# Performance work log

Measured on AMD Instinct MI355X. Metric: run time of the kernel, lower is better.

## Reference

```python
import jax, jax.numpy as jnp
import numpy as np

B, C, H, W = 32, 256, 32, 32
K, HEADS, U, V = 16, 4, 1, 64  # dim_depth, heads, dim_u, dim_v = dim_out//heads
R = 23
PAD = (R - 1) // 2
EPS = 1e-5


def setup_inputs() -> dict:
    key = jax.random.key(0)
    ks = jax.random.split(key, 10)
    return {
        "x": jax.random.normal(ks[0], (B, C, H, W), jnp.float32),
        "Wq": jax.random.normal(ks[1], (K * HEADS, C), jnp.float32) * (1.0 / np.sqrt(C)),
        "bn_q_w": jax.random.uniform(ks[2], (K * HEADS,), jnp.float32, 0.5, 1.5),
        "bn_q_b": jax.random.normal(ks[3], (K * HEADS,), jnp.float32) * 0.1,
        "Wk": jax.random.normal(ks[4], (K * U, C), jnp.float32) * (1.0 / np.sqrt(C)),
        "Wv": jax.random.normal(ks[5], (V * U, C), jnp.float32) * (1.0 / np.sqrt(C)),
        "bn_v_w": jax.random.uniform(ks[6], (V * U,), jnp.float32, 0.5, 1.5),
        "bn_v_b": jax.random.normal(ks[7], (V * U,), jnp.float32) * 0.1,
        "embedding": jax.random.normal(ks[8], (K, U, 1, R, R), jnp.float32),
        "gamma": jax.random.normal(ks[9], (1,), jnp.float32),
    }


def _conv1x1(x, w):
    # x: [b,c,h,w], w: [o,c] -> [b,o,h,w]
    return jnp.einsum('bchw,oc->bohw', x, w)


def _bn(x, w, b):
    # training-mode BatchNorm2d: batch stats over (b,h,w) per channel
    mean = jnp.mean(x, axis=(0, 2, 3), keepdims=True)
    var = jnp.var(x, axis=(0, 2, 3), keepdims=True)
    xn = (x - mean) * jax.lax.rsqrt(var + EPS)
    return xn * w[None, :, None, None] + b[None, :, None, None]


def reference(x, Wq, bn_q_w, bn_q_b, Wk, Wv, bn_v_w, bn_v_b, embedding, gamma):
    b, c, h, w = x.shape
    n = h * w
    queries = _bn(_conv1x1(x, Wq), bn_q_w, bn_q_b).reshape(b, HEADS, K, n)        # bhkn
    softmax = jax.nn.softmax(_conv1x1(x, Wk).reshape(b, K, U, n), axis=-1)         # bkun
    values = _bn(_conv1x1(x, Wv), bn_v_w, bn_v_b).reshape(b, V, U, n)              # bvun

    # content lambda
    lambda_c = jnp.einsum('bkun,bvun->bkv', softmax, values)
    y_c = jnp.einsum('bhkn,bkv->bhvn', queries, lambda_c)

    # position lambda via conv3d over (V, H, W) with kernel (1, R, R)
    v5 = jnp.transpose(values, (0, 2, 1, 3)).reshape(b, U, V, h, w)                # NCDHW, C=U, D=V
    lambda_p = jax.lax.conv_general_dilated(
        v5, embedding,
        window_strides=(1, 1, 1),
        padding=((0, 0), (PAD, PAD), (PAD, PAD)),
        dimension_numbers=('NCDHW', 'OIDHW', 'NCDHW'))                              # [b,K,V,h,w]
    lambda_p = lambda_p.reshape(b, K, V, n)
    y_p = jnp.einsum('bhkn,bkvn->bhvn', queries, lambda_p)

    out = (y_c + y_p).reshape(b, HEADS * V, h, w)
    out = out + gamma * out
    return out
```

## Files before the change

kernel.cpp:

```cpp
#include <hip/hip_runtime.h>
#include <math.h>

#define BB 32
#define CC 256
#define NPIX 1024
#define KD 16
#define NHEADS 4
#define VDIM 64
#define RR 23
#define PADR 11
#define EPSBN 1e-5f
#define NCH 16

typedef short short8v __attribute__((ext_vector_type(8)));
typedef short short4v __attribute__((ext_vector_type(4)));
typedef float floatx4 __attribute__((ext_vector_type(4)));

__device__ __forceinline__ unsigned short f2bf(float f) {
  union { float f; unsigned u; } c; c.f = f;
  unsigned u = c.u;
  return (unsigned short)((u + 0x7FFFu + ((u >> 16) & 1u)) >> 16);
}
__device__ __forceinline__ float bf2f(unsigned short h) {
  union { unsigned u; float f; } c; c.u = ((unsigned)h) << 16;
  return c.f;
}

__global__ __launch_bounds__(256) void k_prep(const float* __restrict__ emb,
    unsigned short* __restrict__ embA,
    const float* __restrict__ Wq, const float* __restrict__ Wk,
    const float* __restrict__ Wv, unsigned short* __restrict__ wA) {
  int bid = blockIdx.x;
  if (bid < 46) {
    int l = bid * 256 + threadIdx.x;
    if (l >= 23 * 16 * 32) return;
    int dr = l >> 9, rem = l & 511;
    int m = rem >> 5, kd = rem & 31;
    unsigned short val = 0;
    if (kd < 23) val = f2bf(emb[(size_t)m * 529 + dr * 23 + kd]);
    embA[l] = val;
  } else {
    int idx = (bid - 46) * 256 + threadIdx.x;
    int j = idx & 7, lane = (idx >> 3) & 63, ks = (idx >> 9) & 7, ot = idx >> 12;
    int o = ot * 16 + (lane & 15);
    int c = ks * 32 + (lane >> 4) * 8 + j;
    const float* src = (o < 64) ? (Wq + (size_t)o * CC)
                     : (o < 80) ? (Wk + (size_t)(o - 64) * CC)
                                : (Wv + (size_t)(o - 80) * CC);
    wA[idx] = f2bf(src[c]);
  }
}

__global__ __launch_bounds__(256) void k_proj(const float* __restrict__ x,
    const unsigned short* __restrict__ wA,
    float* __restrict__ q_pre, float* __restrict__ k_pre, float* __restrict__ v_pre) {
  int b = blockIdx.y;
  int t = threadIdx.x;
  int s = t >> 6;
  int lane = t & 63;
  int nl = lane & 15, quad = lane >> 4;
  int pix = blockIdx.x * 64 + s * 16 + nl;

  const float* xb = x + ((size_t)b * CC) * NPIX + pix;
  const unsigned short* ap = wA + lane * 8;

  floatx4 acc[9];
#pragma unroll
  for (int i = 0; i < 9; ++i) acc[i] = (floatx4){0.f, 0.f, 0.f, 0.f};

#pragma unroll
  for (int ks = 0; ks < 8; ++ks) {
    union { short8v v; unsigned short u[8]; } bb;
    const float* xc = xb + ((size_t)(ks * 32 + quad * 8)) * NPIX;
#pragma unroll
    for (int j = 0; j < 8; ++j) bb.u[j] = f2bf(xc[(size_t)j * NPIX]);
#pragma unroll
    for (int ot = 0; ot < 9; ++ot) {
      short8v af = *(const short8v*)(ap + ((ot * 8 + ks) << 9));
      acc[ot] = __builtin_amdgcn_mfma_f32_16x16x32_bf16(af, bb.v, acc[ot], 0, 0, 0);
    }
  }

#pragma unroll
  for (int ot = 0; ot < 9; ++ot) {
#pragma unroll
    for (int r = 0; r < 4; ++r) {
      int o = ot * 16 + quad * 4 + r;
      float val = acc[ot][r];
      if (o < 64)      q_pre[((size_t)b * 64 + o) * NPIX + pix] = val;
      else if (o < 80) k_pre[((size_t)b * 16 + (o - 64)) * NPIX + pix] = val;
      else             v_pre[((size_t)b * 64 + (o - 80)) * NPIX + pix] = val;
    }
  }
}

__global__ __launch_bounds__(256) void k_bnstats(const float* __restrict__ q_pre,
    const float* __restrict__ v_pre,
    const float* __restrict__ bn_q_w, const float* __restrict__ bn_q_b,
    const float* __restrict__ bn_v_w, const float* __restrict__ bn_v_b,
    float* __restrict__ stats) {
  int ch = blockIdx.x;
  bool isq = ch < 64;
  int c = isq ? ch : ch - 64;
  const float* src = (isq ? q_pre : v_pre) + (size_t)c * NPIX;
  float s = 0.f, ss = 0.f;
  for (int idx = threadIdx.x; idx < BB * NPIX; idx += 256) {
    int bb = idx >> 10, nn = idx & 1023;
    float v = src[(size_t)bb * 64 * NPIX + nn];
    s += v; ss = fmaf(v, v, ss);
  }
#pragma unroll
  for (int off = 32; off > 0; off >>= 1) {
    s += __shfl_down(s, off);
    ss += __shfl_down(ss, off);
  }
  __shared__ float sh[8];
  if ((threadIdx.x & 63) == 0) {
    sh[(threadIdx.x >> 6) * 2] = s;
    sh[(threadIdx.x >> 6) * 2 + 1] = ss;
  }
  __syncthreads();
  if (threadIdx.x == 0) {
    s = sh[0] + sh[2] + sh[4] + sh[6];
    ss = sh[1] + sh[3] + sh[5] + sh[7];
    const float inv = 1.0f / (float)(BB * NPIX);
    float mean = s * inv;
    float var = ss * inv - mean * mean;
    float rstd = rsqrtf(var + EPSBN);
    float w = isq ? bn_q_w[c] : bn_v_w[c];
    float bi = isq ? bn_q_b[c] : bn_v_b[c];
    float scale = rstd * w;
    float shift = bi - mean * scale;
    if (isq) { stats[c] = scale; stats[64 + c] = shift; }
    else     { stats[128 + c] = scale; stats[192 + c] = shift; }
  }
}

__global__ __launch_bounds__(256) void k_nvsm(float* __restrict__ vn,
    const float* __restrict__ stats, float* __restrict__ vnT,
    const float* __restrict__ k_pre, float* __restrict__ p) {
  __shared__ float lds[64 * 65];
  __shared__ float shm[4], shs[4];
  int b = blockIdx.y, bx = blockIdx.x, t = threadIdx.x;
  if (bx < 16) {
    int n0 = bx * 64;
    for (int l = t; l < 4096; l += 256) {
      int o = l >> 6, nn = l & 63;
      size_t a = ((size_t)b * 64 + o) * NPIX + n0 + nn;
      float v = fmaf(vn[a], stats[128 + o], stats[192 + o]);
      vn[a] = v;
      lds[o * 65 + nn] = v;
    }
    __syncthreads();
    for (int l = t; l < 4096; l += 256) {
      int nn = l >> 6, o = l & 63;
      vnT[((size_t)b * NPIX + n0 + nn) * 64 + o] = lds[o * 65 + nn];
    }
  } else {
    int k = bx - 16;
    const float* src = k_pre + ((size_t)b * 16 + k) * NPIX;
    float v[4];
    float mx = -1e30f;
#pragma unroll
    for (int i = 0; i < 4; ++i) { v[i] = src[t + 256 * i]; mx = fmaxf(mx, v[i]); }
#pragma unroll
    for (int off = 32; off > 0; off >>= 1) mx = fmaxf(mx, __shfl_down(mx, off));
    if ((t & 63) == 0) shm[t >> 6] = mx;
    __syncthreads();
    mx = fmaxf(fmaxf(shm[0], shm[1]), fmaxf(shm[2], shm[3]));
    float s = 0.f;
#pragma unroll
    for (int i = 0; i < 4; ++i) { v[i] = __expf(v[i] - mx); s += v[i]; }
#pragma unroll
    for (int off = 32; off > 0; off >>= 1) s += __shfl_down(s, off);
    if ((t & 63) == 0) shs[t >> 6] = s;
    __syncthreads();
    float r = 1.0f / (shs[0] + shs[1] + shs[2] + shs[3]);
    float* dst = p + ((size_t)b * 16 + k) * NPIX;
#pragma unroll
    for (int i = 0; i < 4; ++i) dst[t + 256 * i] = v[i] * r;
  }
}

__global__ __launch_bounds__(256) void k_lambda_p(const float* __restrict__ p,
    const float* __restrict__ vnT, float* __restrict__ lcp) {
  __shared__ float pl[16 * 64];
  int b = blockIdx.y, nc = blockIdx.x, t = threadIdx.x;
  int n0 = nc * 64;
  for (int l = t; l < 1024; l += 256) {
    int k = l >> 6, nn = l & 63;
    pl[l] = p[((size_t)b * 16 + k) * NPIX + n0 + nn];
  }
  __syncthreads();
  int v = t & 63, wg = t >> 6;
  const float* vt = vnT + ((size_t)b * NPIX + n0) * 64 + v;
  float acc[4] = {0.f, 0.f, 0.f, 0.f};
  for (int i = 0; i < 64; ++i) {
    float val = vt[(size_t)i * 64];
#pragma unroll
    for (int j = 0; j < 4; ++j)
      acc[j] = fmaf(pl[(wg * 4 + j) * 64 + i], val, acc[j]);
  }
  float* dst = lcp + ((size_t)(b * NCH + nc) * 16) * 64;
#pragma unroll
  for (int j = 0; j < 4; ++j)
    dst[(size_t)(wg * 4 + j) * 64 + v] = acc[j];
}

#define IMG_RS 68
#define IMG_CS 3728
#define LAM_RS 1032

union KMainLDS {
  short imgc[4 * IMG_CS];
  short lam[16 * LAM_RS];
};

__device__ __forceinline__ short8v ld_win(const short* p) {
  union { short8v s8; short4v s4[2]; } bu;
  bu.s4[0] = *(const short4v*)p;
  bu.s4[1] = *(const short4v*)(p + 4);
  return bu.s8;
}

__global__ __launch_bounds__(256, 3) void k_conv(const float* __restrict__ vn,
    const float* __restrict__ lcp, const unsigned short* __restrict__ embA,
    unsigned short* __restrict__ lamG) {
  __shared__ __align__(16) KMainLDS u;
  __shared__ float lcv[16];
  int b = blockIdx.y, v = blockIdx.x, t = threadIdx.x;

  int4* z4 = (int4*)u.imgc;
  for (int l = t; l < 1864; l += 256) z4[l] = make_int4(0, 0, 0, 0);
  if (t < 16) {
    float s = 0.f;
#pragma unroll
    for (int nc = 0; nc < NCH; ++nc)
      s += lcp[(((size_t)b * NCH + nc) * 16 + t) * 64 + v];
    lcv[t] = s;
  }
  __syncthreads();

  const float* vsrc = vn + ((size_t)b * 64 + v) * NPIX;
  for (int l = t; l < 512; l += 256) {
    int pix = l * 2;
    int y = pix >> 5, xx = pix & 31;
    float2 vv = *(const float2*)(vsrc + pix);
    unsigned short h0 = f2bf(vv.x), h1 = f2bf(vv.y);
#pragma unroll
    for (int s = 0; s < 4; ++s) {
      int base = s * IMG_CS + (y + PADR) * IMG_RS + xx + PADR + s;
      u.imgc[base] = (short)h0;
      u.imgc[base + 1] = (short)h1;
    }
  }
  __syncthreads();

  int lane = t & 63, wv = t >> 6;
  int nl = lane & 15, quad = lane >> 4;
  int y0 = wv * 8;
  int scopy = (4 - (nl & 3)) & 3;
  int colbase = scopy * IMG_CS + nl + quad * 8 + scopy;
  const unsigned short* aptr = embA + nl * 32 + quad * 8;

  floatx4 acc[16];
#pragma unroll
  for (int i = 0; i < 16; ++i) acc[i] = (floatx4){0.f, 0.f, 0.f, 0.f};

  short8v bfrag[8][2];
#pragma unroll
  for (int rr = 0; rr < 8; ++rr) {
    const short* rp = &u.imgc[(y0 + rr) * IMG_RS + colbase];
    bfrag[rr][0] = ld_win(rp);
    bfrag[rr][1] = ld_win(rp + 16);
  }

  short8v a0 = *(const short8v*)aptr;
  short8v a1 = *(const short8v*)(aptr + 512);
#pragma unroll
  for (int dr = 0; dr < RR; ++dr) {
    short8v afrag = a0;
    a0 = a1;
    if (dr < RR - 2) a1 = *(const short8v*)(aptr + (dr + 2) * 512);
#pragma unroll
    for (int rr = 0; rr < 8; ++rr) {
      int slot = (dr + rr) & 7;
      acc[rr * 2 + 0] = __builtin_amdgcn_mfma_f32_16x16x32_bf16(afrag, bfrag[slot][0], acc[rr * 2 + 0], 0, 0, 0);
      acc[rr * 2 + 1] = __builtin_amdgcn_mfma_f32_16x16x32_bf16(afrag, bfrag[slot][1], acc[rr * 2 + 1], 0, 0, 0);
    }
    if (dr < RR - 1) {
      const short* rp = &u.imgc[(y0 + dr + 8) * IMG_RS + colbase];
      int slot = dr & 7;
      bfrag[slot][0] = ld_win(rp);
      bfrag[slot][1] = ld_win(rp + 16);
    }
  }

  __syncthreads();
#pragma unroll
  for (int tt = 0; tt < 16; ++tt) {
    int y = y0 + (tt >> 1), c0 = (tt & 1) << 4;
    int pix = y * 32 + c0 + nl;
#pragma unroll
    for (int r = 0; r < 4; ++r)
      u.lam[(quad * 4 + r) * LAM_RS + pix] = (short)f2bf(acc[tt][r] + lcv[quad * 4 + r]);
  }
  __syncthreads();

  uint4* dst = (uint4*)(lamG + ((size_t)(b * 64 + v)) * 16 * 1024);
  for (int idx = t; idx < 2048; idx += 256) {
    int row = idx >> 7, col = idx & 127;
    dst[row * 128 + col] = *(const uint4*)&u.lam[row * LAM_RS + col * 8];
  }
}

__global__ __launch_bounds__(256) void k_epi2(const unsigned short* __restrict__ lamG,
    const float* __restrict__ q_pre, const float* __restrict__ stats,
    const float* __restrict__ gamma, float* __restrict__ out) {
  __shared__ float qs[64 * 64];
  int b = blockIdx.y, nc = blockIdx.x, z = blockIdx.z, t = threadIdx.x;
  int n0 = nc * 64;
  for (int l = t; l < 4096; l += 256) {
    int o = l >> 6, nn = l & 63;
    qs[l] = fmaf(q_pre[((size_t)b * 64 + o) * NPIX + n0 + nn], stats[o], stats[64 + o]);
  }
  __syncthreads();
  float g1 = 1.0f + gamma[0];
  int p0 = (t & 15) * 4;
  int g = t >> 4;
#pragma unroll
  for (int vi = 0; vi < 2; ++vi) {
    int v = z * 32 + vi * 16 + g;
    const unsigned short* ls = lamG + ((size_t)(b * 64 + v)) * 16 * 1024 + n0 + p0;
    float yacc[4][4];
#pragma unroll
    for (int h = 0; h < 4; ++h)
#pragma unroll
      for (int i = 0; i < 4; ++i) yacc[h][i] = 0.f;
#pragma unroll
    for (int k = 0; k < 16; ++k) {
      uint2 w = *(const uint2*)(ls + k * 1024);
      float l0 = bf2f((unsigned short)(w.x & 0xffffu));
      float l1 = bf2f((unsigned short)(w.x >> 16));
      float l2 = bf2f((unsigned short)(w.y & 0xffffu));
      float l3 = bf2f((unsigned short)(w.y >> 16));
#pragma unroll
      for (int h = 0; h < 4; ++h) {
        const float* qrow = &qs[(h * 16 + k) * 64 + p0];
        yacc[h][0] = fmaf(qrow[0], l0, yacc[h][0]);
        yacc[h][1] = fmaf(qrow[1], l1, yacc[h][1]);
        yacc[h][2] = fmaf(qrow[2], l2, yacc[h][2]);
        yacc[h][3] = fmaf(qrow[3], l3, yacc[h][3]);
      }
    }
#pragma unroll
    for (int h = 0; h < 4; ++h) {
      float4 r;
      r.x = g1 * yacc[h][0]; r.y = g1 * yacc[h][1];
      r.z = g1 * yacc[h][2]; r.w = g1 * yacc[h][3];
      *(float4*)&out[((size_t)b * 256 + h * 64 + v) * NPIX + n0 + p0] = r;
    }
  }
}

__global__ __launch_bounds__(256, 3) void k_fused(const float* __restrict__ vn,
    const float* __restrict__ q_pre, const float* __restrict__ stats,
    const float* __restrict__ lcp, const unsigned short* __restrict__ embA,
    const float* __restrict__ gamma, float* __restrict__ out) {
  __shared__ __align__(16) KMainLDS u;
  __shared__ float lcv[16];
  int b = blockIdx.y, v = blockIdx.x, t = threadIdx.x;

  int4* z4 = (int4*)u.imgc;
  for (int l = t; l < 1864; l += 256) z4[l] = make_int4(0, 0, 0, 0);
  if (t < 16) {
    float s = 0.f;
#pragma unroll
    for (int nc = 0; nc < NCH; ++nc)
      s += lcp[(((size_t)b * NCH + nc) * 16 + t) * 64 + v];
    lcv[t] = s;
  }
  __syncthreads();

  const float* vsrc = vn + ((size_t)b * 64 + v) * NPIX;
  for (int l = t; l < 512; l += 256) {
    int pix = l * 2;
    int y = pix >> 5, xx = pix & 31;
    float2 vv = *(const float2*)(vsrc + pix);
    unsigned short h0 = f2bf(vv.x), h1 = f2bf(vv.y);
#pragma unroll
    for (int s = 0; s < 4; ++s) {
      int base = s * IMG_CS + (y + PADR) * IMG_RS + xx + PADR + s;
      u.imgc[base] = (short)h0;
      u.imgc[base + 1] = (short)h1;
    }
  }
  __syncthreads();

  int lane = t & 63, wv = t >> 6;
  int nl = lane & 15, quad = lane >> 4;
  int y0 = wv * 8;
  int scopy = (4 - (nl & 3)) & 3;
  int colbase = scopy * IMG_CS + nl + quad * 8 + scopy;
  const unsigned short* aptr = embA + nl * 32 + quad * 8;

  floatx4 acc[16];
#pragma unroll
  for (int i = 0; i < 16; ++i) acc[i] = (floatx4){0.f, 0.f, 0.f, 0.f};

  short8v bfrag[8][2];
#pragma unroll
  for (int rr = 0; rr < 8; ++rr) {
    const short* rp = &u.imgc[(y0 + rr) * IMG_RS + colbase];
    bfrag[rr][0] = ld_win(rp);
    bfrag[rr][1] = ld_win(rp + 16);
  }

  short8v a0 = *(const short8v*)aptr;
  short8v a1 = *(const short8v*)(aptr + 512);
#pragma unroll
  for (int dr = 0; dr < RR; ++dr) {
    short8v afrag = a0;
    a0 = a1;
    if (dr < RR - 2) a1 = *(const short8v*)(aptr + (dr + 2) * 512);
#pragma unroll
    for (int rr = 0; rr < 8; ++rr) {
      int slot = (dr + rr) & 7;
      acc[rr * 2 + 0] = __builtin_amdgcn_mfma_f32_16x16x32_bf16(afrag, bfrag[slot][0], acc[rr * 2 + 0], 0, 0, 0);
      acc[rr * 2 + 1] = __builtin_amdgcn_mfma_f32_16x16x32_bf16(afrag, bfrag[slot][1], acc[rr * 2 + 1], 0, 0, 0);
    }
    if (dr < RR - 1) {
      const short* rp = &u.imgc[(y0 + dr + 8) * IMG_RS + colbase];
      int slot = dr & 7;
      bfrag[slot][0] = ld_win(rp);
      bfrag[slot][1] = ld_win(rp + 16);
    }
  }

  __syncthreads();
#pragma unroll
  for (int tt = 0; tt < 16; ++tt) {
    int y = y0 + (tt >> 1), c0 = (tt & 1) << 4;
    int pix = y * 32 + c0 + nl;
#pragma unroll
    for (int r = 0; r < 4; ++r)
      u.lam[(quad * 4 + r) * LAM_RS + pix] = (short)f2bf(acc[tt][r] + lcv[quad * 4 + r]);
  }
  __syncthreads();

  int p0 = t * 4;
  float yacc[4][4];
#pragma unroll
  for (int h = 0; h < 4; ++h)
#pragma unroll
    for (int i = 0; i < 4; ++i) yacc[h][i] = 0.f;
  const float* qb = q_pre + ((size_t)b * 64) * NPIX + p0;
#pragma unroll
  for (int k = 0; k < 16; ++k) {
    uint2 w = *(const uint2*)&u.lam[k * LAM_RS + p0];
    float l0 = bf2f((unsigned short)(w.x & 0xffffu));
    float l1 = bf2f((unsigned short)(w.x >> 16));
    float l2 = bf2f((unsigned short)(w.y & 0xffffu));
    float l3 = bf2f((unsigned short)(w.y >> 16));
#pragma unroll
    for (int h = 0; h < 4; ++h) {
      int o = h * 16 + k;
      float4 qv = *(const float4*)(qb + (size_t)o * NPIX);
      float s = stats[o], sh = stats[64 + o];
      yacc[h][0] = fmaf(fmaf(qv.x, s, sh), l0, yacc[h][0]);
      yacc[h][1] = fmaf(fmaf(qv.y, s, sh), l1, yacc[h][1]);
      yacc[h][2] = fmaf(fmaf(qv.z, s, sh), l2, yacc[h][2]);
      yacc[h][3] = fmaf(fmaf(qv.w, s, sh), l3, yacc[h][3]);
    }
  }
  float g1 = 1.0f + gamma[0];
#pragma unroll
  for (int h = 0; h < 4; ++h) {
    float4 r;
    r.x = g1 * yacc[h][0]; r.y = g1 * yacc[h][1];
    r.z = g1 * yacc[h][2]; r.w = g1 * yacc[h][3];
    *(float4*)&out[((size_t)b * 256 + h * 64 + v) * NPIX + p0] = r;
  }
}

extern "C" void kernel_launch(void* const* d_in, const int* in_sizes, int n_in,
                              void* d_out, int out_size, void* d_ws, size_t ws_size,
                              hipStream_t stream) {
  const float* x      = (const float*)d_in[0];
  const float* Wq     = (const float*)d_in[1];
  const float* bn_q_w = (const float*)d_in[2];
  const float* bn_q_b = (const float*)d_in[3];
  const float* Wk     = (const float*)d_in[4];
  const float* Wv     = (const float*)d_in[5];
  const float* bn_v_w = (const float*)d_in[6];
  const float* bn_v_b = (const float*)d_in[7];
  const float* emb    = (const float*)d_in[8];
  const float* gamma  = (const float*)d_in[9];
  float* out = (float*)d_out;

  float* ws    = (float*)d_ws;
  float* q_pre = ws;
  float* k_pre = q_pre + (size_t)BB * 64 * NPIX;
  float* vn    = k_pre + (size_t)BB * 16 * NPIX;
  float* vnT   = vn    + (size_t)BB * 64 * NPIX;
  float* p     = vnT   + (size_t)BB * NPIX * 64;
  float* lcp   = p     + (size_t)BB * 16 * NPIX;
  float* stats = lcp   + (size_t)BB * NCH * 16 * 64;
  unsigned short* embA = (unsigned short*)(stats + 256);
  unsigned short* wA   = embA + 23 * 16 * 32;
  unsigned short* lamG = wA + 144 * 256;

  size_t need = ((size_t)(lamG - (unsigned short*)ws)) * 2
              + (size_t)BB * 64 * 16 * NPIX * 2;

  k_prep    <<<dim3(190),     256, 0, stream>>>(emb, embA, Wq, Wk, Wv, wA);
  k_proj    <<<dim3(16, BB),  256, 0, stream>>>(x, wA, q_pre, k_pre, vn);
  k_bnstats <<<dim3(128),     256, 0, stream>>>(q_pre, vn, bn_q_w, bn_q_b, bn_v_w, bn_v_b, stats);
  k_nvsm    <<<dim3(32, BB),  256, 0, stream>>>(vn, stats, vnT, k_pre, p);
  k_lambda_p<<<dim3(NCH, BB), 256, 0, stream>>>(p, vnT, lcp);
  if (ws_size >= need) {
    k_conv  <<<dim3(64, BB),    256, 0, stream>>>(vn, lcp, embA, lamG);
    k_epi2  <<<dim3(16, BB, 2), 256, 0, stream>>>(lamG, q_pre, stats, gamma, out);
  } else {
    k_fused <<<dim3(64, BB),    256, 0, stream>>>(vn, q_pre, stats, lcp, embA, gamma, out);
  }
}
```

Before: 228.7 us.

## Fuse BN statistics into projection and content lambda into conv, drop transposes

```diff
diff --git a/kernel.cpp b/kernel.cpp
--- a/kernel.cpp
+++ b/kernel.cpp
@@ -10,7 +10,6 @@
 #define RR 23
 #define PADR 11
 #define EPSBN 1e-5f
-#define NCH 16
 
 typedef short short8v __attribute__((ext_vector_type(8)));
 typedef short short4v __attribute__((ext_vector_type(4)));
@@ -26,11 +25,15 @@
   return c.f;
 }
 
+#define NINV (1.0f / 32768.0f)
+
 __global__ __launch_bounds__(256) void k_prep(const float* __restrict__ emb,
     unsigned short* __restrict__ embA,
     const float* __restrict__ Wq, const float* __restrict__ Wk,
-    const float* __restrict__ Wv, unsigned short* __restrict__ wA) {
+    const float* __restrict__ Wv, unsigned short* __restrict__ wA,
+    float* __restrict__ raw) {
   int bid = blockIdx.x;
+  if (bid == 0) raw[threadIdx.x] = 0.f;
   if (bid < 46) {
     int l = bid * 256 + threadIdx.x;
     if (l >= 23 * 16 * 32) return;
@@ -53,7 +56,9 @@
 
 __global__ __launch_bounds__(256) void k_proj(const float* __restrict__ x,
     const unsigned short* __restrict__ wA,
-    float* __restrict__ q_pre, float* __restrict__ k_pre, float* __restrict__ v_pre) {
+    float* __restrict__ q_pre, float* __restrict__ k_pre, float* __restrict__ v_pre,
+    float* __restrict__ raw) {
+  __shared__ float ssum[144], ssq[144];
   int b = blockIdx.y;
   int t = threadIdx.x;
   int s = t >> 6;
@@ -61,6 +66,9 @@
   int nl = lane & 15, quad = lane >> 4;
   int pix = blockIdx.x * 64 + s * 16 + nl;
 
+  if (t < 144) { ssum[t] = 0.f; ssq[t] = 0.f; }
+  __syncthreads();
+
   const float* xb = x + ((size_t)b * CC) * NPIX + pix;
   const unsigned short* ap = wA + lane * 8;
 
@@ -92,69 +100,57 @@
       else             v_pre[((size_t)b * 64 + (o - 80)) * NPIX + pix] = val;
     }
   }
-}
-
-__global__ __launch_bounds__(256) void k_bnstats(const float* __restrict__ q_pre,
-    const float* __restrict__ v_pre,
-    const float* __restrict__ bn_q_w, const float* __restrict__ bn_q_b,
+
+#pragma unroll
+  for (int ot = 0; ot < 9; ++ot) {
+#pragma unroll
+    for (int r = 0; r < 4; ++r) {
+      int o = ot * 16 + quad * 4 + r;
+      if (o >= 64 && o < 80) continue;
+      float v1 = acc[ot][r];
+      float v2 = v1 * v1;
+#pragma unroll
+      for (int m = 1; m < 16; m <<= 1) {
+        v1 += __shfl_xor(v1, m);
+        v2 += __shfl_xor(v2, m);
+      }
+      if (nl == 0) {
+        atomicAdd(&ssum[o], v1);
+        atomicAdd(&ssq[o], v2);
+      }
+    }
+  }
+  __syncthreads();
+  if (t < 64) {
+    atomicAdd(&raw[t], ssum[t]);
+    atomicAdd(&raw[64 + t], ssq[t]);
+  } else if (t < 128) {
+    atomicAdd(&raw[64 + t], ssum[t + 16]);
+    atomicAdd(&raw[192 + (t - 64)], ssq[t + 16]);
+  }
+}
+
+__global__ __launch_bounds__(256) void k_nvsm(float* __restrict__ vn,
+    const float* __restrict__ raw,
     const float* __restrict__ bn_v_w, const float* __restrict__ bn_v_b,
-    float* __restrict__ stats) {
-  int ch = blockIdx.x;
-  bool isq = ch < 64;
-  int c = isq ? ch : ch - 64;
-  const float* src = (isq ? q_pre : v_pre) + (size_t)c * NPIX;
-  float s = 0.f, ss = 0.f;
-  for (int idx = threadIdx.x; idx < BB * NPIX; idx += 256) {
-    int bb = idx >> 10, nn = idx & 1023;
-    float v = src[(size_t)bb * 64 * NPIX + nn];
-    s += v; ss = fmaf(v, v, ss);
-  }
-#pragma unroll
-  for (int off = 32; off > 0; off >>= 1) {
-    s += __shfl_down(s, off);
-    ss += __shfl_down(ss, off);
-  }
-  __shared__ float sh[8];
-  if ((threadIdx.x & 63) == 0) {
-    sh[(threadIdx.x >> 6) * 2] = s;
-    sh[(threadIdx.x >> 6) * 2 + 1] = ss;
-  }
-  __syncthreads();
-  if (threadIdx.x == 0) {
-    s = sh[0] + sh[2] + sh[4] + sh[6];
-    ss = sh[1] + sh[3] + sh[5] + sh[7];
-    const float inv = 1.0f / (float)(BB * NPIX);
-    float mean = s * inv;
-    float var = ss * inv - mean * mean;
-    float rstd = rsqrtf(var + EPSBN);
-    float w = isq ? bn_q_w[c] : bn_v_w[c];
-    float bi = isq ? bn_q_b[c] : bn_v_b[c];
-    float scale = rstd * w;
-    float shift = bi - mean * scale;
-    if (isq) { stats[c] = scale; stats[64 + c] = shift; }
-    else     { stats[128 + c] = scale; stats[192 + c] = shift; }
-  }
-}
-
-__global__ __launch_bounds__(256) void k_nvsm(float* __restrict__ vn,
-    const float* __restrict__ stats, float* __restrict__ vnT,
     const float* __restrict__ k_pre, float* __restrict__ p) {
-  __shared__ float lds[64 * 65];
+  __shared__ float vsc[64], vsh[64];
   __shared__ float shm[4], shs[4];
   int b = blockIdx.y, bx = blockIdx.x, t = threadIdx.x;
   if (bx < 16) {
+    if (t < 64) {
+      float mean = raw[128 + t] * NINV;
+      float var = raw[192 + t] * NINV - mean * mean;
+      float sc = rsqrtf(var + EPSBN) * bn_v_w[t];
+      vsc[t] = sc;
+      vsh[t] = bn_v_b[t] - mean * sc;
+    }
+    __syncthreads();
     int n0 = bx * 64;
     for (int l = t; l < 4096; l += 256) {
       int o = l >> 6, nn = l & 63;
       size_t a = ((size_t)b * 64 + o) * NPIX + n0 + nn;
-      float v = fmaf(vn[a], stats[128 + o], stats[192 + o]);
-      vn[a] = v;
-      lds[o * 65 + nn] = v;
-    }
-    __syncthreads();
-    for (int l = t; l < 4096; l += 256) {
-      int nn = l >> 6, o = l & 63;
-      vnT[((size_t)b * NPIX + n0 + nn) * 64 + o] = lds[o * 65 + nn];
+      vn[a] = fmaf(vn[a], vsc[o], vsh[o]);
     }
   } else {
     int k = bx - 16;
@@ -182,31 +178,6 @@
   }
 }
 
-__global__ __launch_bounds__(256) void k_lambda_p(const float* __restrict__ p,
-    const float* __restrict__ vnT, float* __restrict__ lcp) {
-  __shared__ float pl[16 * 64];
-  int b = blockIdx.y, nc = blockIdx.x, t = threadIdx.x;
-  int n0 = nc * 64;
-  for (int l = t; l < 1024; l += 256) {
-    int k = l >> 6, nn = l & 63;
-    pl[l] = p[((size_t)b * 16 + k) * NPIX + n0 + nn];
-  }
-  __syncthreads();
-  int v = t & 63, wg = t >> 6;
-  const float* vt = vnT + ((size_t)b * NPIX + n0) * 64 + v;
-  float acc[4] = {0.f, 0.f, 0.f, 0.f};
-  for (int i = 0; i < 64; ++i) {
-    float val = vt[(size_t)i * 64];
-#pragma unroll
-    for (int j = 0; j < 4; ++j)
-      acc[j] = fmaf(pl[(wg * 4 + j) * 64 + i], val, acc[j]);
-  }
-  float* dst = lcp + ((size_t)(b * NCH + nc) * 16) * 64;
-#pragma unroll
-  for (int j = 0; j < 4; ++j)
-    dst[(size_t)(wg * 4 + j) * 64 + v] = acc[j];
-}
-
 #define IMG_RS 68
 #define IMG_CS 3728
 #define LAM_RS 1032
@@ -224,22 +195,32 @@
 }
 
 __global__ __launch_bounds__(256, 3) void k_conv(const float* __restrict__ vn,
-    const float* __restrict__ lcp, const unsigned short* __restrict__ embA,
+    const float* __restrict__ p, const unsigned short* __restrict__ embA,
     unsigned short* __restrict__ lamG) {
   __shared__ __align__(16) KMainLDS u;
   __shared__ float lcv[16];
+  __shared__ float red[256];
   int b = blockIdx.y, v = blockIdx.x, t = threadIdx.x;
 
   int4* z4 = (int4*)u.imgc;
   for (int l = t; l < 1864; l += 256) z4[l] = make_int4(0, 0, 0, 0);
+
+  {
+    int kk = t & 15, ch = t >> 4;
+    const float* pp = p + ((size_t)b * 16 + kk) * NPIX + ch * 64;
+    const float* vv = vn + ((size_t)b * 64 + v) * NPIX + ch * 64;
+    float part = 0.f;
+#pragma unroll 8
+    for (int i = 0; i < 64; ++i) part = fmaf(pp[i], vv[i], part);
+    red[t] = part;
+  }
+  __syncthreads();
   if (t < 16) {
     float s = 0.f;
 #pragma unroll
-    for (int nc = 0; nc < NCH; ++nc)
-      s += lcp[(((size_t)b * NCH + nc) * 16 + t) * 64 + v];
+    for (int c = 0; c < 16; ++c) s += red[c * 16 + t];
     lcv[t] = s;
   }
-  __syncthreads();
 
   const float* vsrc = vn + ((size_t)b * 64 + v) * NPIX;
   for (int l = t; l < 512; l += 256) {
@@ -315,14 +296,24 @@
 }
 
 __global__ __launch_bounds__(256) void k_epi2(const unsigned short* __restrict__ lamG,
-    const float* __restrict__ q_pre, const float* __restrict__ stats,
+    const float* __restrict__ q_pre, const float* __restrict__ raw,
+    const float* __restrict__ bn_q_w, const float* __restrict__ bn_q_b,
     const float* __restrict__ gamma, float* __restrict__ out) {
   __shared__ float qs[64 * 64];
+  __shared__ float qsc[64], qsh[64];
   int b = blockIdx.y, nc = blockIdx.x, z = blockIdx.z, t = threadIdx.x;
+  if (t < 64) {
+    float mean = raw[t] * NINV;
+    float var = raw[64 + t] * NINV - mean * mean;
+    float sc = rsqrtf(var + EPSBN) * bn_q_w[t];
+    qsc[t] = sc;
+    qsh[t] = bn_q_b[t] - mean * sc;
+  }
+  __syncthreads();
   int n0 = nc * 64;
   for (int l = t; l < 4096; l += 256) {
     int o = l >> 6, nn = l & 63;
-    qs[l] = fmaf(q_pre[((size_t)b * 64 + o) * NPIX + n0 + nn], stats[o], stats[64 + o]);
+    qs[l] = fmaf(q_pre[((size_t)b * 64 + o) * NPIX + n0 + nn], qsc[o], qsh[o]);
   }
   __syncthreads();
   float g1 = 1.0f + gamma[0];
@@ -364,23 +355,41 @@
 }
 
 __global__ __launch_bounds__(256, 3) void k_fused(const float* __restrict__ vn,
-    const float* __restrict__ q_pre, const float* __restrict__ stats,
-    const float* __restrict__ lcp, const unsigned short* __restrict__ embA,
+    const float* __restrict__ q_pre, const float* __restrict__ raw,
+    const float* __restrict__ bn_q_w, const float* __restrict__ bn_q_b,
+    const float* __restrict__ p, const unsigned short* __restrict__ embA,
     const float* __restrict__ gamma, float* __restrict__ out) {
   __shared__ __align__(16) KMainLDS u;
   __shared__ float lcv[16];
+  __shared__ float red[256];
+  __shared__ float qsc[64], qsh[64];
   int b = blockIdx.y, v = blockIdx.x, t = threadIdx.x;
 
   int4* z4 = (int4*)u.imgc;
   for (int l = t; l < 1864; l += 256) z4[l] = make_int4(0, 0, 0, 0);
+  if (t < 64) {
+    float mean = raw[t] * NINV;
+    float var = raw[64 + t] * NINV - mean * mean;
+    float sc = rsqrtf(var + EPSBN) * bn_q_w[t];
+    qsc[t] = sc;
+    qsh[t] = bn_q_b[t] - mean * sc;
+  }
+  {
+    int kk = t & 15, ch = t >> 4;
+    const float* pp = p + ((size_t)b * 16 + kk) * NPIX + ch * 64;
+    const float* vv = vn + ((size_t)b * 64 + v) * NPIX + ch * 64;
+    float part = 0.f;
+#pragma unroll 8
+    for (int i = 0; i < 64; ++i) part = fmaf(pp[i], vv[i], part);
+    red[t] = part;
+  }
+  __syncthreads();
   if (t < 16) {
     float s = 0.f;
 #pragma unroll
-    for (int nc = 0; nc < NCH; ++nc)
-      s += lcp[(((size_t)b * NCH + nc) * 16 + t) * 64 + v];
+    for (int c = 0; c < 16; ++c) s += red[c * 16 + t];
     lcv[t] = s;
   }
-  __syncthreads();
 
   const float* vsrc = vn + ((size_t)b * 64 + v) * NPIX;
   for (int l = t; l < 512; l += 256) {
@@ -466,11 +475,10 @@
     for (int h = 0; h < 4; ++h) {
       int o = h * 16 + k;
       float4 qv = *(const float4*)(qb + (size_t)o * NPIX);
-      float s = stats[o], sh = stats[64 + o];
-      yacc[h][0] = fmaf(fmaf(qv.x, s, sh), l0, yacc[h][0]);
-      yacc[h][1] = fmaf(fmaf(qv.y, s, sh), l1, yacc[h][1]);
-      yacc[h][2] = fmaf(fmaf(qv.z, s, sh), l2, yacc[h][2]);
-      yacc[h][3] = fmaf(fmaf(qv.w, s, sh), l3, yacc[h][3]);
+      yacc[h][0] = fmaf(fmaf(qv.x, qsc[o], qsh[o]), l0, yacc[h][0]);
+      yacc[h][1] = fmaf(fmaf(qv.y, qsc[o], qsh[o]), l1, yacc[h][1]);
+      yacc[h][2] = fmaf(fmaf(qv.z, qsc[o], qsh[o]), l2, yacc[h][2]);
+      yacc[h][3] = fmaf(fmaf(qv.w, qsc[o], qsh[o]), l3, yacc[h][3]);
     }
   }
   float g1 = 1.0f + gamma[0];
@@ -502,26 +510,22 @@
   float* q_pre = ws;
   float* k_pre = q_pre + (size_t)BB * 64 * NPIX;
   float* vn    = k_pre + (size_t)BB * 16 * NPIX;
-  float* vnT   = vn    + (size_t)BB * 64 * NPIX;
-  float* p     = vnT   + (size_t)BB * NPIX * 64;
-  float* lcp   = p     + (size_t)BB * 16 * NPIX;
-  float* stats = lcp   + (size_t)BB * NCH * 16 * 64;
-  unsigned short* embA = (unsigned short*)(stats + 256);
+  float* p     = vn    + (size_t)BB * 64 * NPIX;
+  float* raw   = p     + (size_t)BB * 16 * NPIX;
+  unsigned short* embA = (unsigned short*)(raw + 256);
   unsigned short* wA   = embA + 23 * 16 * 32;
   unsigned short* lamG = wA + 144 * 256;
 
   size_t need = ((size_t)(lamG - (unsigned short*)ws)) * 2
               + (size_t)BB * 64 * 16 * NPIX * 2;
 
-  k_prep    <<<dim3(190),     256, 0, stream>>>(emb, embA, Wq, Wk, Wv, wA);
-  k_proj    <<<dim3(16, BB),  256, 0, stream>>>(x, wA, q_pre, k_pre, vn);
-  k_bnstats <<<dim3(128),     256, 0, stream>>>(q_pre, vn, bn_q_w, bn_q_b, bn_v_w, bn_v_b, stats);
-  k_nvsm    <<<dim3(32, BB),  256, 0, stream>>>(vn, stats, vnT, k_pre, p);
-  k_lambda_p<<<dim3(NCH, BB), 256, 0, stream>>>(p, vnT, lcp);
+  k_prep  <<<dim3(190),       256, 0, stream>>>(emb, embA, Wq, Wk, Wv, wA, raw);
+  k_proj  <<<dim3(16, BB),    256, 0, stream>>>(x, wA, q_pre, k_pre, vn, raw);
+  k_nvsm  <<<dim3(32, BB),    256, 0, stream>>>(vn, raw, bn_v_w, bn_v_b, k_pre, p);
   if (ws_size >= need) {
-    k_conv  <<<dim3(64, BB),    256, 0, stream>>>(vn, lcp, embA, lamG);
-    k_epi2  <<<dim3(16, BB, 2), 256, 0, stream>>>(lamG, q_pre, stats, gamma, out);
+    k_conv<<<dim3(64, BB),    256, 0, stream>>>(vn, p, embA, lamG);
+    k_epi2<<<dim3(16, BB, 2), 256, 0, stream>>>(lamG, q_pre, raw, bn_q_w, bn_q_b, gamma, out);
   } else {
-    k_fused <<<dim3(64, BB),    256, 0, stream>>>(vn, q_pre, stats, lcp, embA, gamma, out);
-  }
-}
+    k_fused<<<dim3(64, BB),   256, 0, stream>>>(vn, q_pre, raw, bn_q_w, bn_q_b, p, embA, gamma, out);
+  }
+}
```

Measured after the change: 214.6 us. 1.07x faster.
